# Performance work log

Measured on AMD Instinct MI355X. Metric: run time of the kernel, lower is better.

Reference implementation:

```python
import jax, jax.numpy as jnp
import numpy as np

B, S, HID = 1, 4096, 2048
NH, NKV, HD = 16, 4, 128
BLK, LOCAL, GNB, STRIDE = 64, 4, 2, 4
ROT = 64  # head_dim * rope_partial_rotary_factor(0.5), already even
SCALE = HD ** -0.5
NEG = -1e9


def _block_select(nb):
    """Static local+global key-block selection per query block (mirrors _select_key_blocks)."""
    sels = []
    for bi in range(nb):
        local = list(range(max(0, bi - LOCAL + 1), bi + 1))
        gc = list(range(0, bi + 1, STRIDE))
        if len(gc) > GNB:
            gc = gc[-GNB:]
        if 0 not in gc:
            gc = [0] + gc
        idx = sorted(set(local + gc))
        sels.append([i for i in idx if 0 <= i < nb and i <= bi])
    m = max(len(s) for s in sels)
    idx = np.zeros((nb, m), np.int32)
    valid = np.zeros((nb, m), bool)
    for i, s in enumerate(sels):
        idx[i, :len(s)] = s
        valid[i, :len(s)] = True
    return jnp.asarray(idx), jnp.asarray(valid)


def _rot_half(x):
    h = x.shape[-1] // 2
    return jnp.concatenate([-x[..., h:], x[..., :h]], axis=-1)


def setup_inputs() -> dict:
    key = jax.random.key(0)
    ks = jax.random.split(key, 8)
    w = lambda k, shp: (jax.random.normal(k, shp, jnp.float32) * 0.02)
    return {
        "hidden": jax.random.normal(ks[0], (B, S, HID), jnp.float32),
        "cos": jax.random.uniform(ks[1], (B, S, ROT), jnp.float32, -1.0, 1.0),
        "sin": jax.random.uniform(ks[2], (B, S, ROT), jnp.float32, -1.0, 1.0),
        "Wq": w(ks[3], (HID, NH * HD)),
        "Wk": w(ks[4], (HID, NKV * HD)),
        "Wv": w(ks[5], (HID, NKV * HD)),
        "Wo": w(ks[6], (NH * HD, HID)),
        "attn_mask": jnp.ones((B, S), jnp.float32),
    }


def reference(hidden, cos, sin, Wq, Wk, Wv, Wo, attn_mask):
    b_, s_, _ = hidden.shape
    q = (hidden @ Wq).reshape(b_, s_, NH, HD).transpose(0, 2, 1, 3)   # [B,H,S,d]
    k = (hidden @ Wk).reshape(b_, s_, NKV, HD).transpose(0, 2, 1, 3)  # [B,Hkv,S,d]
    v = (hidden @ Wv).reshape(b_, s_, NKV, HD).transpose(0, 2, 1, 3)

    # partial RoPE on first ROT channels
    c = cos[:, None, :, :]
    sn = sin[:, None, :, :]
    q1, q2 = q[..., :ROT], q[..., ROT:]
    k1, k2 = k[..., :ROT], k[..., ROT:]
    q = jnp.concatenate([q1 * c + _rot_half(q1) * sn, q2], axis=-1)
    k = jnp.concatenate([k1 * c + _rot_half(k1) * sn, k2], axis=-1)

    # repeat_kv (GQA expand: each kv head repeated contiguously)
    rep = NH // NKV
    k = jnp.repeat(k, rep, axis=1)
    v = jnp.repeat(v, rep, axis=1)

    nb = s_ // BLK  # S chosen divisible by BLK (pad_len == 0)
    qb = q.reshape(b_, NH, nb, BLK, HD)
    kb = k.reshape(b_, NH, nb, BLK, HD)
    vb = v.reshape(b_, NH, nb, BLK, HD)

    idx, valid = _block_select(nb)  # [nb, M]
    m = idx.shape[1]
    ksel = kb[:, :, idx]  # [B,H,nb,M,BLK,d]
    vsel = vb[:, :, idx]

    scores = jnp.einsum('bhnqd,bhnmkd->bhnqmk',
                        qb.astype(jnp.float32), ksel.astype(jnp.float32)) * SCALE
    # key-validity (padding) mask, additive as in original
    key_valid = attn_mask.reshape(b_, nb, BLK)
    kvm = key_valid[:, idx]  # [B,nb,M,BLK]
    scores = scores + (1.0 - kvm[:, None, :, None, :, :]) * NEG
    # invalid (padded) selected slots
    scores = jnp.where(valid[None, None, :, None, :, None], scores, NEG)
    # intra-block causal mask on the diagonal block
    intra = jnp.triu(jnp.ones((BLK, BLK), bool), 1)                    # [q,k]
    same = idx == jnp.arange(nb)[:, None]                              # [nb,M]
    diag = same[:, None, :, None] & intra[None, :, None, :]            # [nb,q,M,k]
    scores = jnp.where(diag[None, None], NEG, scores)

    probs = jax.nn.softmax(scores.reshape(b_, NH, nb, BLK, m * BLK), axis=-1)
    vflat = vsel.reshape(b_, NH, nb, m * BLK, HD)
    out = jnp.einsum('bhnqe,bhned->bhnqd', probs.astype(v.dtype), vflat)
    out = out.reshape(b_, NH, s_, HD).transpose(0, 2, 1, 3).reshape(b_, s_, NH * HD)
    return out @ Wo
```

## Files before the change

### kernel.cpp

```cpp
#include <hip/hip_runtime.h>
#include <hip/hip_bf16.h>


typedef short short8 __attribute__((ext_vector_type(8)));
typedef float f32x4  __attribute__((ext_vector_type(4)));

#define NEGV   (-1.0e9f)
#define SCALE  (0.08838834764831845f)

__device__ __forceinline__ void gload16(const void* g, void* l) {
  __builtin_amdgcn_global_load_lds(
      (const __attribute__((address_space(1))) unsigned int*)g,
      (__attribute__((address_space(3))) unsigned int*)l, 16, 0, 0);
}

__device__ __forceinline__ float bf2f(short s) {
  union { unsigned u; float f; } c;
  c.u = ((unsigned)(unsigned short)s) << 16;
  return c.f;
}

__device__ __forceinline__ short f2bf_s(float f) {
  __hip_bfloat16 b = __float2bfloat16(f);
  short s;
  __builtin_memcpy(&s, &b, 2);
  return s;
}

__global__ void prep_all(const float* __restrict__ H, const float* __restrict__ Wq,
                         const float* __restrict__ Wk, const float* __restrict__ Wv,
                         const float* __restrict__ Wo, __hip_bfloat16* __restrict__ X,
                         __hip_bfloat16* __restrict__ Wt, __hip_bfloat16* __restrict__ Wot) {
  __shared__ short tile[64][73];
  const int b = blockIdx.x;
  const int tid = threadIdx.x;
  if (b < 4096) {
    size_t t = (size_t)b * 256 + tid;
    const float* hp = H + t * 8;
    float4 v0 = *(const float4*)hp;
    float4 v1 = *(const float4*)(hp + 4);
    short8 o;
    o[0] = f2bf_s(v0.x); o[1] = f2bf_s(v0.y); o[2] = f2bf_s(v0.z); o[3] = f2bf_s(v0.w);
    o[4] = f2bf_s(v1.x); o[5] = f2bf_s(v1.y); o[6] = f2bf_s(v1.z); o[7] = f2bf_s(v1.w);
    *(short8*)&X[t * 8] = o;
    return;
  }
  const float* src; __hip_bfloat16* dst; int C; int idx;
  int q = b - 4096;
  if (q < 1024)      { src = Wq; dst = Wt;                       C = 2048; idx = q; }
  else if (q < 1280) { src = Wk; dst = Wt + (size_t)2048 * 2048; C = 512;  idx = q - 1024; }
  else if (q < 1536) { src = Wv; dst = Wt + (size_t)2560 * 2048; C = 512;  idx = q - 1280; }
  else               { src = Wo; dst = Wot;                      C = 2048; idx = q - 1536; }
  const int r0 = (idx & 31) * 64, c0 = (idx >> 5) * 64;
  const int c4 = (tid & 15) * 4, rb = tid >> 4;
#pragma unroll
  for (int j = 0; j < 4; ++j) {
    int r = rb + j * 16;
    float4 v = *(const float4*)(src + (size_t)(r0 + r) * C + c0 + c4);
    tile[r][c4 + 0] = f2bf_s(v.x);
    tile[r][c4 + 1] = f2bf_s(v.y);
    tile[r][c4 + 2] = f2bf_s(v.z);
    tile[r][c4 + 3] = f2bf_s(v.w);
  }
  __syncthreads();
  const int cs = (tid & 7) * 8;
#pragma unroll
  for (int it = 0; it < 2; ++it) {
    int cc = (tid >> 3) + it * 32;
    short8 o;
#pragma unroll
    for (int i = 0; i < 8; ++i) o[i] = tile[cs + i][cc];
    *(short8*)&dst[(size_t)(c0 + cc) * 2048 + r0 + cs] = o;
  }
}

__global__ void postproc(const float* __restrict__ cosb, const float* __restrict__ sinb,
                         __hip_bfloat16* __restrict__ Kb,
                         const __hip_bfloat16* __restrict__ Vb, __hip_bfloat16* __restrict__ Vt) {
  __shared__ __hip_bfloat16 tile[64][73];
  int blk = blockIdx.x;
  if (blk < 256) {
    int tk = blk * 256 + threadIdx.x;
    int s = tk >> 4;
    int rem = tk & 15;
    __hip_bfloat16* p = Kb + (size_t)s * 512 + (rem >> 2) * 128 + (rem & 3) * 8;
    const int g8 = (tk & 3) * 8;
    const float* cp = cosb + (size_t)s * 64 + g8;
    const float* sp = sinb + (size_t)s * 64 + g8;
    short8 a = *(const short8*)p;
    short8 b = *(const short8*)(p + 32);
    float ca[8], sa[8], cb[8], sb[8];
    *(float4*)&ca[0] = *(const float4*)cp;        *(float4*)&ca[4] = *(const float4*)(cp + 4);
    *(float4*)&cb[0] = *(const float4*)(cp + 32); *(float4*)&cb[4] = *(const float4*)(cp + 36);
    *(float4*)&sa[0] = *(const float4*)sp;        *(float4*)&sa[4] = *(const float4*)(sp + 4);
    *(float4*)&sb[0] = *(const float4*)(sp + 32); *(float4*)&sb[4] = *(const float4*)(sp + 36);
    short8 oa, ob;
#pragma unroll
    for (int i = 0; i < 8; ++i) {
      float av = bf2f(a[i]), bv = bf2f(b[i]);
      oa[i] = f2bf_s(av * ca[i] - bv * sa[i]);
      ob[i] = f2bf_s(bv * cb[i] + av * sb[i]);
    }
    *(short8*)p = oa;
    *(short8*)(p + 32) = ob;
    return;
  }
  int idx = blk - 256;
  int s0 = (idx & 63) * 64, c0 = (idx >> 6) * 64;
  int c = threadIdx.x & 63, rq = threadIdx.x >> 6;
#pragma unroll
  for (int i = 0; i < 16; ++i) {
    int r = i * 4 + rq;
    tile[r][c] = Vb[(size_t)(s0 + r) * 512 + c0 + c];
  }
  __syncthreads();
#pragma unroll
  for (int i = 0; i < 16; ++i) {
    int cc = i * 4 + rq;
    Vt[(size_t)(c0 + cc) * 4096 + s0 + c] = tile[c][cc];
  }
}

__global__ __launch_bounds__(512, 2) void gemm_qkv2p(
    const __hip_bfloat16* __restrict__ A, const __hip_bfloat16* __restrict__ Bt,
    __hip_bfloat16* __restrict__ Qb, __hip_bfloat16* __restrict__ Kb,
    __hip_bfloat16* __restrict__ Vb) {
  const int K = 2048;
  const int tid = threadIdx.x;
  const int wave = tid >> 6, lane = tid & 63;
  const int l15 = lane & 15, lg = lane >> 4;
  const int bm = blockIdx.x, bn = blockIdx.y;
  const int wm = wave >> 2, wn = wave & 3;

  __shared__ __hip_bfloat16 lds[57344];

  f32x4 acc[8][3] = {};
  const int srow = lane >> 3;
  const int sslot = lane & 7;
  const int scol = (sslot ^ srow) * 8;
  const size_t abase = (size_t)bm * 256 * K;
  const size_t bbase = (size_t)bn * 192 * K;
  const int r3 = l15 & 7;

#define STAGE_A(HALF, KO, LBASE)                                                 \
  {                                                                              \
    _Pragma("unroll")                                                            \
    for (int l = 0; l < 2; ++l) {                                                \
      int chunk = l * 8 + wave;                                                  \
      int row = chunk * 8 + srow;                                                \
      gload16(A + abase + (size_t)((HALF) * 128 + row) * K + (KO) + scol,        \
              &lds[(LBASE) + chunk * 512]);                                      \
    }                                                                            \
  }
#define STAGE_B(KO, LBASE)                                                       \
  {                                                                              \
    _Pragma("unroll")                                                            \
    for (int l = 0; l < 3; ++l) {                                                \
      int chunk = l * 8 + wave;                                                  \
      int row = chunk * 8 + srow;                                                \
      gload16(Bt + bbase + (size_t)row * K + (KO) + scol,                        \
              &lds[(LBASE) + chunk * 512]);                                      \
    }                                                                            \
  }

  short8 bfr[3][2];
  short8 af[2][2][2];

#define READ_AF(P, Q, BA)                                                        \
  {                                                                              \
    _Pragma("unroll")                                                            \
    for (int m2 = 0; m2 < 2; ++m2)                                               \
      _Pragma("unroll")                                                          \
      for (int ks = 0; ks < 2; ++ks) {                                           \
        int row = ((Q) * 2 + m2) * 16 + l15;                                     \
        int slot = (ks * 4 + lg) ^ r3;                                           \
        af[P][m2][ks] = *(const short8*)&lds[(BA) + row * 64 + slot * 8];        \
      }                                                                          \
  }

#define READ_BF(BB)                                                              \
  {                                                                              \
    _Pragma("unroll")                                                            \
    for (int ni = 0; ni < 3; ++ni)                                               \
      _Pragma("unroll")                                                          \
      for (int ks = 0; ks < 2; ++ks) {                                           \
        int row = wn * 48 + ni * 16 + l15;                                       \
        int slot = (ks * 4 + lg) ^ r3;                                           \
        bfr[ni][ks] = *(const short8*)&lds[(BB) + row * 64 + slot * 8];          \
      }                                                                          \
  }

#define MFMA_2Q(QA, QB)                                                          \
  {                                                                              \
    __builtin_amdgcn_s_setprio(1);                                               \
    _Pragma("unroll")                                                            \
    for (int ks = 0; ks < 2; ++ks)                                               \
      _Pragma("unroll")                                                          \
      for (int m2 = 0; m2 < 2; ++m2)                                             \
        _Pragma("unroll")                                                        \
        for (int ni = 0; ni < 3; ++ni) {                                         \
          acc[(QA) * 2 + m2][ni] = __builtin_amdgcn_mfma_f32_16x16x32_bf16(      \
              af[0][m2][ks], bfr[ni][ks], acc[(QA) * 2 + m2][ni], 0, 0, 0);      \
          acc[(QB) * 2 + m2][ni] = __builtin_amdgcn_mfma_f32_16x16x32_bf16(      \
              af[1][m2][ks], bfr[ni][ks], acc[(QB) * 2 + m2][ni], 0, 0, 0);      \
        }                                                                        \
    __builtin_amdgcn_s_setprio(0);                                               \
  }

#define LGKM0()                                                                  \
  asm volatile("s_waitcnt lgkmcnt(0)" ::: "memory");                             \
  __builtin_amdgcn_sched_barrier(0);

  STAGE_B(0, 16384);
  STAGE_A(0, 0, 0);
  STAGE_A(1, 0, 8192);
  STAGE_B(64, 28672 + 16384);
  asm volatile("s_waitcnt vmcnt(3)" ::: "memory");
  __builtin_amdgcn_sched_barrier(0);
  __builtin_amdgcn_s_barrier();
  {
    READ_BF(16384);
    READ_AF(0, 0, wm * 8192);
    READ_AF(1, 1, wm * 8192);
  }
  LGKM0();

  for (int t = 0; t < 32; ++t) {
    const int buf = (t & 1) * 28672;
    const int nbuf = buf ^ 28672;
    const int bA = buf + wm * 8192;
    if (t + 1 < 32) { STAGE_A(0, (t + 1) * 64, nbuf); STAGE_A(1, (t + 1) * 64, nbuf + 8192); }
    __builtin_amdgcn_s_barrier();
    MFMA_2Q(0, 1);
    READ_AF(0, 2, bA);
    READ_AF(1, 3, bA);
    LGKM0();
    if (t + 2 < 32) STAGE_B((t + 2) * 64, buf + 16384);
    if (t < 30) asm volatile("s_waitcnt vmcnt(3)" ::: "memory");
    else        asm volatile("s_waitcnt vmcnt(0)" ::: "memory");
    __builtin_amdgcn_sched_barrier(0);
    __builtin_amdgcn_s_barrier();
    MFMA_2Q(2, 3);
    if (t + 1 < 32) {
      READ_BF(nbuf + 16384);
      READ_AF(0, 0, nbuf + wm * 8192);
      READ_AF(1, 1, nbuf + wm * 8192);
    }
    LGKM0();
  }
#undef STAGE_A
#undef STAGE_B
#undef READ_AF
#undef READ_BF
#undef MFMA_2Q
#undef LGKM0

#pragma unroll
  for (int m8 = 0; m8 < 8; ++m8)
#pragma unroll
    for (int ni = 0; ni < 3; ++ni) {
      int colg = bn * 192 + wn * 48 + ni * 16;
      __hip_bfloat16* dst; int ldc, col;
      if (colg < 2048)      { dst = Qb; ldc = 2048; col = colg + l15; }
      else if (colg < 2560) { dst = Kb; ldc = 512;  col = colg - 2048 + l15; }
      else                  { dst = Vb; ldc = 512;  col = colg - 2560 + l15; }
      int row = bm * 256 + wm * 128 + m8 * 16 + lg * 4;
#pragma unroll
      for (int r = 0; r < 4; ++r)
        dst[(size_t)(row + r) * ldc + col] = __float2bfloat16(acc[m8][ni][r]);
    }
}

__global__ __launch_bounds__(256) void gemm_bt(
    const __hip_bfloat16* __restrict__ A, const __hip_bfloat16* __restrict__ Bt,
    float* __restrict__ C, int M, int N, int K) {
  const int tid = threadIdx.x;
  const int wave = tid >> 6, lane = tid & 63;
  const int l15 = lane & 15, lg = lane >> 4;
  const int bm = blockIdx.x, bn = blockIdx.y;
  const int wm = wave >> 1, wn = wave & 1;

  __shared__ __hip_bfloat16 As[128 * 64];
  __shared__ __hip_bfloat16 Bs[128 * 64];

  f32x4 acc[4][4] = {};
  const int lrow = lane >> 3;
  const int lslot = lane & 7;
  const int scol = (lslot ^ lrow) * 8;
  const size_t abase = (size_t)bm * 128 * K;
  const size_t bbase = (size_t)bn * 128 * K;
  const int r3 = l15 & 7;

  for (int k0 = 0; k0 < K; k0 += 64) {
#pragma unroll
    for (int i = 0; i < 4; ++i) {
      int seg = i * 4 + wave;
      int row = seg * 8 + lrow;
      gload16(A + abase + (size_t)row * K + k0 + scol, &As[seg * 512]);
      gload16(Bt + bbase + (size_t)row * K + k0 + scol, &Bs[seg * 512]);
    }
    __syncthreads();
#pragma unroll
    for (int ks = 0; ks < 2; ++ks) {
      const int slot = (ks * 4 + lg) ^ r3;
      short8 af[4], bf[4];
#pragma unroll
      for (int mi = 0; mi < 4; ++mi)
        af[mi] = *(const short8*)&As[(wm * 64 + mi * 16 + l15) * 64 + slot * 8];
#pragma unroll
      for (int ni = 0; ni < 4; ++ni)
        bf[ni] = *(const short8*)&Bs[(wn * 64 + ni * 16 + l15) * 64 + slot * 8];
#pragma unroll
      for (int mi = 0; mi < 4; ++mi)
#pragma unroll
        for (int ni = 0; ni < 4; ++ni)
          acc[mi][ni] = __builtin_amdgcn_mfma_f32_16x16x32_bf16(af[mi], bf[ni], acc[mi][ni], 0, 0, 0);
    }
    __syncthreads();
  }
#pragma unroll
  for (int mi = 0; mi < 4; ++mi)
#pragma unroll
    for (int ni = 0; ni < 4; ++ni) {
      int row = bm * 128 + wm * 64 + mi * 16 + lg * 4;
      int col = bn * 128 + wn * 64 + ni * 16 + l15;
#pragma unroll
      for (int r = 0; r < 4; ++r)
        C[(size_t)(row + r) * N + col] = acc[mi][ni][r];
    }
}

__global__ __launch_bounds__(512, 2) void attn_kernel(
    const __hip_bfloat16* __restrict__ Qb,
    const __hip_bfloat16* __restrict__ Kb,
    const __hip_bfloat16* __restrict__ Vt,
    const float* __restrict__ cosb, const float* __restrict__ sinb,
    const float* __restrict__ amask,
    __hip_bfloat16* __restrict__ AO)
{
  const int bid = blockIdx.x;
  const int kvh = bid & 3;
  const int bi  = bid >> 2;
  const int tid = threadIdx.x;
  const int wave = tid >> 6, lane = tid & 63;
  const int l15 = lane & 15, lg = lane >> 4;
  const int h  = kvh * 4 + (wave >> 1);
  const int rh = wave & 1;
  const int q0 = bi * 64 + rh * 32;

  int sel[6]; int nsel = 0;
  {
    int gtop = bi >> 2;
    for (int j = 0; j <= bi; ++j) {
      bool pick = (j == 0) || (j >= bi - 3) || (((j & 3) == 0) && ((j >> 2) >= gtop - 1));
      if (pick && nsel < 6) sel[nsel++] = j;
    }
  }

  __shared__ __hip_bfloat16 kv[2][16384];
  __shared__ __hip_bfloat16 Pl[8][2304];

  short8 qf[2][4];
#pragma unroll
  for (int mi = 0; mi < 2; ++mi) {
    const int s_ = q0 + mi * 16 + l15;
    const __hip_bfloat16* qrow = Qb + (size_t)s_ * 2048 + h * 128;
#pragma unroll
    for (int ks = 0; ks < 4; ++ks)
      qf[mi][ks] = *(const short8*)(qrow + ks * 32 + lg * 8);
    const float* cp = cosb + (size_t)s_ * 64 + lg * 8;
    const float* sp = sinb + (size_t)s_ * 64 + lg * 8;
    float ca[8], sa[8], cb[8], sb[8];
    *(float4*)&ca[0] = *(const float4*)cp;        *(float4*)&ca[4] = *(const float4*)(cp + 4);
    *(float4*)&cb[0] = *(const float4*)(cp + 32); *(float4*)&cb[4] = *(const float4*)(cp + 36);
    *(float4*)&sa[0] = *(const float4*)sp;        *(float4*)&sa[4] = *(const float4*)(sp + 4);
    *(float4*)&sb[0] = *(const float4*)(sp + 32); *(float4*)&sb[4] = *(const float4*)(sp + 36);
    short8 a = qf[mi][0], b = qf[mi][1], oa, ob;
#pragma unroll
    for (int i = 0; i < 8; ++i) {
      float av = bf2f(a[i]), bv = bf2f(b[i]);
      oa[i] = f2bf_s(av * ca[i] - bv * sa[i]);
      ob[i] = f2bf_s(bv * cb[i] + av * sb[i]);
    }
    qf[mi][0] = oa;
    qf[mi][1] = ob;
  }

  float m[2][4], l[2][4];
  f32x4 oacc[2][8] = {};
#pragma unroll
  for (int mi = 0; mi < 2; ++mi)
#pragma unroll
    for (int r = 0; r < 4; ++r) { m[mi][r] = -3.0e38f; l[mi][r] = 0.f; }

#define STAGE_KV(KB, BUF)                                                          \
  {                                                                                \
    _Pragma("unroll")                                                              \
    for (int i = 0; i < 2; ++i) {                                                  \
      int chunk = (i * 8 + wave) * 64 + lane;                                      \
      int row = chunk >> 4, slot = chunk & 15;                                     \
      gload16(Kb + (size_t)((KB) * 64 + row) * 512 + kvh * 128 +                   \
                  ((slot ^ (row & 15)) * 8),                                       \
              &kv[BUF][(i * 8 + wave) * 512]);                                     \
    }                                                                              \
    _Pragma("unroll")                                                              \
    for (int i = 0; i < 2; ++i) {                                                  \
      int chunk = (i * 8 + wave) * 64 + lane;                                      \
      int row = chunk >> 3, slot = chunk & 7;                                      \
      gload16(Vt + (size_t)(kvh * 128 + row) * 4096 + (KB) * 64 +                  \
                  ((slot ^ (row & 7)) * 8),                                        \
              &kv[BUF][8192 + (i * 8 + wave) * 512]);                              \
    }                                                                              \
  }

  STAGE_KV(sel[0], 0);

#pragma unroll
  for (int j = 0; j < 6; ++j) {
    if (j < nsel) {
      const int kb = sel[j];
      if (j + 1 < nsel) {
        STAGE_KV(sel[j + 1], (j + 1) & 1);
        asm volatile("s_waitcnt vmcnt(4)" ::: "memory");
      } else {
        asm volatile("s_waitcnt vmcnt(0)" ::: "memory");
      }
      __builtin_amdgcn_sched_barrier(0);
      __builtin_amdgcn_s_barrier();
      const __hip_bfloat16* kbuf = kv[j & 1];

      f32x4 sc[2][4] = {};
#pragma unroll
      for (int nf = 0; nf < 4; ++nf)
#pragma unroll
        for (int ks = 0; ks < 4; ++ks) {
          short8 b = *(const short8*)&kbuf[(nf * 16 + l15) * 128 +
                                           (((ks * 4 + lg) ^ l15) * 8)];
          sc[0][nf] = __builtin_amdgcn_mfma_f32_16x16x32_bf16(qf[0][ks], b, sc[0][nf], 0, 0, 0);
          sc[1][nf] = __builtin_amdgcn_mfma_f32_16x16x32_bf16(qf[1][ks], b, sc[1][nf], 0, 0, 0);
        }

      float am[4];
#pragma unroll
      for (int nf = 0; nf < 4; ++nf)
        am[nf] = (1.0f - amask[kb * 64 + nf * 16 + l15]) * NEGV;
#pragma unroll
      for (int mi = 0; mi < 2; ++mi)
#pragma unroll
        for (int nf = 0; nf < 4; ++nf) {
          int keyl = nf * 16 + l15;
#pragma unroll
          for (int r = 0; r < 4; ++r) {
            float s = sc[mi][nf][r] * SCALE + am[nf];
            if (kb == bi) {
              int qrow = rh * 32 + mi * 16 + lg * 4 + r;
              if (keyl > qrow) s = NEGV;
            }
            sc[mi][nf][r] = s;
          }
        }

      float pm[2][4];
#pragma unroll
      for (int mi = 0; mi < 2; ++mi)
#pragma unroll
        for (int r = 0; r < 4; ++r) {
          float v = fmaxf(fmaxf(sc[mi][0][r], sc[mi][1][r]),
                          fmaxf(sc[mi][2][r], sc[mi][3][r]));
          v = fmaxf(v, __shfl_xor(v, 1)); v = fmaxf(v, __shfl_xor(v, 2));
          v = fmaxf(v, __shfl_xor(v, 4)); v = fmaxf(v, __shfl_xor(v, 8));
          pm[mi][r] = v;
        }

      bool need = false;
#pragma unroll
      for (int mi = 0; mi < 2; ++mi)
#pragma unroll
        for (int r = 0; r < 4; ++r) need |= (pm[mi][r] - m[mi][r] > 8.0f);
      if (__any(need)) {
#pragma unroll
        for (int mi = 0; mi < 2; ++mi)
#pragma unroll
          for (int r = 0; r < 4; ++r) {
            float mn = fmaxf(m[mi][r], pm[mi][r]);
            float scl = __expf(m[mi][r] - mn);
            l[mi][r] *= scl;
#pragma unroll
            for (int df = 0; df < 8; ++df) oacc[mi][df][r] *= scl;
            m[mi][r] = mn;
          }
      }

#pragma unroll
      for (int mi = 0; mi < 2; ++mi)
#pragma unroll
        for (int r = 0; r < 4; ++r) {
          float rs = 0.f;
#pragma unroll
          for (int nf = 0; nf < 4; ++nf) {
            float p = __expf(sc[mi][nf][r] - m[mi][r]);
            rs += p;
            Pl[wave][(mi * 16 + lg * 4 + r) * 72 + nf * 16 + l15] = __float2bfloat16(p);
          }
          rs += __shfl_xor(rs, 1); rs += __shfl_xor(rs, 2);
          rs += __shfl_xor(rs, 4); rs += __shfl_xor(rs, 8);
          l[mi][r] += rs;
        }

      short8 af2[2][2];
#pragma unroll
      for (int mi = 0; mi < 2; ++mi)
#pragma unroll
        for (int ks = 0; ks < 2; ++ks)
          af2[mi][ks] = *(const short8*)&Pl[wave][(mi * 16 + l15) * 72 + ks * 32 + lg * 8];
#pragma unroll
      for (int df = 0; df < 8; ++df)
#pragma unroll
        for (int ks = 0; ks < 2; ++ks) {
          short8 vb = *(const short8*)&kbuf[8192 + (df * 16 + l15) * 64 +
                                            (((ks * 4 + lg) ^ (l15 & 7)) * 8)];
          oacc[0][df] = __builtin_amdgcn_mfma_f32_16x16x32_bf16(af2[0][ks], vb, oacc[0][df], 0, 0, 0);
          oacc[1][df] = __builtin_amdgcn_mfma_f32_16x16x32_bf16(af2[1][ks], vb, oacc[1][df], 0, 0, 0);
        }
      __builtin_amdgcn_s_barrier();
    }
  }
#undef STAGE_KV

#pragma unroll
  for (int mi = 0; mi < 2; ++mi) {
    float inv[4];
#pragma unroll
    for (int r = 0; r < 4; ++r) inv[r] = 1.0f / l[mi][r];
#pragma unroll
    for (int df = 0; df < 8; ++df)
#pragma unroll
      for (int r = 0; r < 4; ++r) {
        int qrow = q0 + mi * 16 + lg * 4 + r;
        AO[(size_t)qrow * 2048 + h * 128 + df * 16 + l15] =
            __float2bfloat16(oacc[mi][df][r] * inv[r]);
      }
  }
}

extern "C" void kernel_launch(void* const* d_in, const int* in_sizes, int n_in,
                              void* d_out, int out_size, void* d_ws, size_t ws_size,
                              hipStream_t stream) {
  const float* hidden = (const float*)d_in[0];
  const float* cosb   = (const float*)d_in[1];
  const float* sinb   = (const float*)d_in[2];
  const float* Wq     = (const float*)d_in[3];
  const float* Wk     = (const float*)d_in[4];
  const float* Wv     = (const float*)d_in[5];
  const float* Wo     = (const float*)d_in[6];
  const float* amask  = (const float*)d_in[7];

  char* ws = (char*)d_ws;
  __hip_bfloat16* Xb   = (__hip_bfloat16*)(ws);
  __hip_bfloat16* Wt   = (__hip_bfloat16*)(ws + 16777216);
  __hip_bfloat16* Wot  = (__hip_bfloat16*)(ws + 29360128);
  __hip_bfloat16* Qb   = (__hip_bfloat16*)(ws + 37748736);
  __hip_bfloat16* Kb   = (__hip_bfloat16*)(ws + 54525952);
  __hip_bfloat16* Vb   = (__hip_bfloat16*)(ws + 58720256);
  __hip_bfloat16* Vt   = (__hip_bfloat16*)(ws + 62914560);
  __hip_bfloat16* AO   = Xb;

  prep_all<<<6656, 256, 0, stream>>>(hidden, Wq, Wk, Wv, Wo, Xb, Wt, Wot);

  gemm_qkv2p<<<dim3(16, 16), 512, 0, stream>>>(Xb, Wt, Qb, Kb, Vb);

  postproc<<<768, 256, 0, stream>>>(cosb, sinb, Kb, Vb, Vt);

  attn_kernel<<<256, 512, 0, stream>>>(Qb, Kb, Vt, cosb, sinb, amask, AO);

  gemm_bt<<<dim3(32, 16), 256, 0, stream>>>(AO, Wot, (float*)d_out, 4096, 2048, 2048);
}
```

Before: 155.3 us.

## Replace output GEMM with double-buffered 256x128 pipelined MFMA kernel

Replaces the simple single-buffered 128x128 output-projection GEMM with a 512-thread, 256x128-tile kernel modeled on the QKV GEMM. It double-buffers A and B in LDS and interleaves global-to-LDS staging with MFMA quadrants using split barriers, waitcnt control and setprio. The goal is to hide global load latency and raise reuse per tile. The cost is more LDS (96KB) and more register pressure, and the grid halves to 256 blocks, which may underfill the CUs.

```diff
diff --git a/kernel.cpp b/kernel.cpp
--- a/kernel.cpp
+++ b/kernel.cpp
@@ -250,10 +250,6 @@
   }
 #undef STAGE_A
 #undef STAGE_B
-#undef READ_AF
-#undef READ_BF
-#undef MFMA_2Q
-#undef LGKM0
 
 #pragma unroll
   for (int m8 = 0; m8 < 8; ++m8)
@@ -269,64 +265,154 @@
       for (int r = 0; r < 4; ++r)
         dst[(size_t)(row + r) * ldc + col] = __float2bfloat16(acc[m8][ni][r]);
     }
-}
-
-__global__ __launch_bounds__(256) void gemm_bt(
+#undef READ_AF
+#undef READ_BF
+#undef MFMA_2Q
+#undef LGKM0
+}
+
+__global__ __launch_bounds__(512, 2) void gemm_out2p(
     const __hip_bfloat16* __restrict__ A, const __hip_bfloat16* __restrict__ Bt,
-    float* __restrict__ C, int M, int N, int K) {
+    float* __restrict__ C) {
+  const int K = 2048, N = 2048;
   const int tid = threadIdx.x;
   const int wave = tid >> 6, lane = tid & 63;
   const int l15 = lane & 15, lg = lane >> 4;
   const int bm = blockIdx.x, bn = blockIdx.y;
-  const int wm = wave >> 1, wn = wave & 1;
-
-  __shared__ __hip_bfloat16 As[128 * 64];
-  __shared__ __hip_bfloat16 Bs[128 * 64];
-
-  f32x4 acc[4][4] = {};
-  const int lrow = lane >> 3;
-  const int lslot = lane & 7;
-  const int scol = (lslot ^ lrow) * 8;
-  const size_t abase = (size_t)bm * 128 * K;
+  const int wm = wave >> 2, wn = wave & 3;
+
+  __shared__ __hip_bfloat16 lds[49152];
+
+  f32x4 acc[8][2] = {};
+  const int srow = lane >> 3;
+  const int sslot = lane & 7;
+  const int scol = (sslot ^ srow) * 8;
+  const size_t abase = (size_t)bm * 256 * K;
   const size_t bbase = (size_t)bn * 128 * K;
   const int r3 = l15 & 7;
 
-  for (int k0 = 0; k0 < K; k0 += 64) {
-#pragma unroll
-    for (int i = 0; i < 4; ++i) {
-      int seg = i * 4 + wave;
-      int row = seg * 8 + lrow;
-      gload16(A + abase + (size_t)row * K + k0 + scol, &As[seg * 512]);
-      gload16(Bt + bbase + (size_t)row * K + k0 + scol, &Bs[seg * 512]);
-    }
-    __syncthreads();
-#pragma unroll
-    for (int ks = 0; ks < 2; ++ks) {
-      const int slot = (ks * 4 + lg) ^ r3;
-      short8 af[4], bf[4];
-#pragma unroll
-      for (int mi = 0; mi < 4; ++mi)
-        af[mi] = *(const short8*)&As[(wm * 64 + mi * 16 + l15) * 64 + slot * 8];
-#pragma unroll
-      for (int ni = 0; ni < 4; ++ni)
-        bf[ni] = *(const short8*)&Bs[(wn * 64 + ni * 16 + l15) * 64 + slot * 8];
-#pragma unroll
-      for (int mi = 0; mi < 4; ++mi)
-#pragma unroll
-        for (int ni = 0; ni < 4; ++ni)
-          acc[mi][ni] = __builtin_amdgcn_mfma_f32_16x16x32_bf16(af[mi], bf[ni], acc[mi][ni], 0, 0, 0);
-    }
-    __syncthreads();
-  }
-#pragma unroll
-  for (int mi = 0; mi < 4; ++mi)
-#pragma unroll
-    for (int ni = 0; ni < 4; ++ni) {
-      int row = bm * 128 + wm * 64 + mi * 16 + lg * 4;
-      int col = bn * 128 + wn * 64 + ni * 16 + l15;
+#define STAGE_A(HALF, KO, LBASE)                                                 \
+  {                                                                              \
+    _Pragma("unroll")                                                            \
+    for (int l = 0; l < 2; ++l) {                                                \
+      int chunk = l * 8 + wave;                                                  \
+      int row = chunk * 8 + srow;                                                \
+      gload16(A + abase + (size_t)((HALF) * 128 + row) * K + (KO) + scol,        \
+              &lds[(LBASE) + chunk * 512]);                                      \
+    }                                                                            \
+  }
+#define STAGE_B(KO, LBASE)                                                       \
+  {                                                                              \
+    _Pragma("unroll")                                                            \
+    for (int l = 0; l < 2; ++l) {                                                \
+      int chunk = l * 8 + wave;                                                  \
+      int row = chunk * 8 + srow;                                                \
+      gload16(Bt + bbase + (size_t)row * K + (KO) + scol,                        \
+              &lds[(LBASE) + chunk * 512]);                                      \
+    }                                                                            \
+  }
+
+  short8 bfr[2][2];
+  short8 af[2][2][2];
+
+#define READ_AF(P, Q, BA)                                                        \
+  {                                                                              \
+    _Pragma("unroll")                                                            \
+    for (int m2 = 0; m2 < 2; ++m2)                                               \
+      _Pragma("unroll")                                                          \
+      for (int ks = 0; ks < 2; ++ks) {                                           \
+        int row = ((Q) * 2 + m2) * 16 + l15;                                     \
+        int slot = (ks * 4 + lg) ^ r3;                                           \
+        af[P][m2][ks] = *(const short8*)&lds[(BA) + row * 64 + slot * 8];        \
+      }                                                                          \
+  }
+
+#define READ_BF(BB)                                                              \
+  {                                                                              \
+    _Pragma("unroll")                                                            \
+    for (int ni = 0; ni < 2; ++ni)                                               \
+      _Pragma("unroll")                                                          \
+      for (int ks = 0; ks < 2; ++ks) {                                           \
+        int row = wn * 32 + ni * 16 + l15;                                       \
+        int slot = (ks * 4 + lg) ^ r3;                                           \
+        bfr[ni][ks] = *(const short8*)&lds[(BB) + row * 64 + slot * 8];          \
+      }                                                                          \
+  }
+
+#define MFMA_2Q(QA, QB)                                                          \
+  {                                                                              \
+    __builtin_amdgcn_s_setprio(1);                                               \
+    _Pragma("unroll")                                                            \
+    for (int ks = 0; ks < 2; ++ks)                                               \
+      _Pragma("unroll")                                                          \
+      for (int m2 = 0; m2 < 2; ++m2)                                             \
+        _Pragma("unroll")                                                        \
+        for (int ni = 0; ni < 2; ++ni) {                                         \
+          acc[(QA) * 2 + m2][ni] = __builtin_amdgcn_mfma_f32_16x16x32_bf16(      \
+              af[0][m2][ks], bfr[ni][ks], acc[(QA) * 2 + m2][ni], 0, 0, 0);      \
+          acc[(QB) * 2 + m2][ni] = __builtin_amdgcn_mfma_f32_16x16x32_bf16(      \
+              af[1][m2][ks], bfr[ni][ks], acc[(QB) * 2 + m2][ni], 0, 0, 0);      \
+        }                                                                        \
+    __builtin_amdgcn_s_setprio(0);                                               \
+  }
+
+#define LGKM0()                                                                  \
+  asm volatile("s_waitcnt lgkmcnt(0)" ::: "memory");                             \
+  __builtin_amdgcn_sched_barrier(0);
+
+  STAGE_B(0, 16384);
+  STAGE_A(0, 0, 0);
+  STAGE_A(1, 0, 8192);
+  STAGE_B(64, 24576 + 16384);
+  asm volatile("s_waitcnt vmcnt(2)" ::: "memory");
+  __builtin_amdgcn_sched_barrier(0);
+  __builtin_amdgcn_s_barrier();
+  {
+    READ_BF(16384);
+    READ_AF(0, 0, wm * 8192);
+    READ_AF(1, 1, wm * 8192);
+  }
+  LGKM0();
+
+  for (int t = 0; t < 32; ++t) {
+    const int buf = (t & 1) * 24576;
+    const int nbuf = buf ^ 24576;
+    const int bA = buf + wm * 8192;
+    if (t + 1 < 32) { STAGE_A(0, (t + 1) * 64, nbuf); STAGE_A(1, (t + 1) * 64, nbuf + 8192); }
+    __builtin_amdgcn_s_barrier();
+    MFMA_2Q(0, 1);
+    READ_AF(0, 2, bA);
+    READ_AF(1, 3, bA);
+    LGKM0();
+    if (t + 2 < 32) STAGE_B((t + 2) * 64, buf + 16384);
+    if (t < 30) asm volatile("s_waitcnt vmcnt(2)" ::: "memory");
+    else        asm volatile("s_waitcnt vmcnt(0)" ::: "memory");
+    __builtin_amdgcn_sched_barrier(0);
+    __builtin_amdgcn_s_barrier();
+    MFMA_2Q(2, 3);
+    if (t + 1 < 32) {
+      READ_BF(nbuf + 16384);
+      READ_AF(0, 0, nbuf + wm * 8192);
+      READ_AF(1, 1, nbuf + wm * 8192);
+    }
+    LGKM0();
+  }
+#undef STAGE_A
+#undef STAGE_B
+#undef READ_AF
+#undef READ_BF
+#undef MFMA_2Q
+#undef LGKM0
+
+#pragma unroll
+  for (int m8 = 0; m8 < 8; ++m8)
+#pragma unroll
+    for (int ni = 0; ni < 2; ++ni) {
+      int row = bm * 256 + wm * 128 + m8 * 16 + lg * 4;
+      int col = bn * 128 + wn * 32 + ni * 16 + l15;
 #pragma unroll
       for (int r = 0; r < 4; ++r)
-        C[(size_t)(row + r) * N + col] = acc[mi][ni][r];
+        C[(size_t)(row + r) * N + col] = acc[m8][ni][r];
     }
 }
 
@@ -573,5 +659,5 @@
 
   attn_kernel<<<256, 512, 0, stream>>>(Qb, Kb, Vt, cosb, sinb, amask, AO);
 
-  gemm_bt<<<dim3(32, 16), 256, 0, stream>>>(AO, Wot, (float*)d_out, 4096, 2048, 2048);
-}
+  gemm_out2p<<<dim3(16, 16), 512, 0, stream>>>(AO, Wot, (float*)d_out);
+}
```

Result: faster. 150.1 us (-3.3%).
